# Optimization experiments

Measured on AMD Instinct MI355X. Metric: run time of the kernel, lower is better.

The kernel has to match this reference:

```python
import math
import jax, jax.numpy as jnp
import numpy as np

NUM_LAYERS = 4
D_MODEL = 1024
N_HEAD = 8
HEAD_DIM = D_MODEL // N_HEAD
B, L = 8, 512
EPS = 1e-5


def setup_inputs() -> dict:
    key = jax.random.key(0)
    ks = jax.random.split(key, 6)
    x = jax.random.normal(ks[0], (B, L, D_MODEL), dtype=jnp.float32)
    mask = jnp.ones((B, L), dtype=jnp.int32)
    qv_w = jax.random.normal(ks[1], (NUM_LAYERS, 2 * D_MODEL, D_MODEL), dtype=jnp.float32) * 0.02
    r_r_bias = jax.random.normal(ks[2], (NUM_LAYERS, N_HEAD, HEAD_DIM), dtype=jnp.float32) * 0.02
    r_w_bias = jax.random.normal(ks[3], (NUM_LAYERS, N_HEAD, HEAD_DIM), dtype=jnp.float32) * 0.02
    ffn_w = jax.random.normal(ks[4], (NUM_LAYERS, D_MODEL, D_MODEL), dtype=jnp.float32) * 0.02
    ffn_b = jnp.zeros((NUM_LAYERS, D_MODEL), dtype=jnp.float32)
    ln1_g = jnp.ones((NUM_LAYERS, D_MODEL), dtype=jnp.float32)
    ln1_b = jnp.zeros((NUM_LAYERS, D_MODEL), dtype=jnp.float32)
    ln2_g = jnp.ones((NUM_LAYERS, D_MODEL), dtype=jnp.float32)
    ln2_b = jnp.zeros((NUM_LAYERS, D_MODEL), dtype=jnp.float32)
    return dict(x=x, mask=mask, qv_w=qv_w, r_r_bias=r_r_bias, r_w_bias=r_w_bias,
                ln1_g=ln1_g, ln1_b=ln1_b, ffn_w=ffn_w, ffn_b=ffn_b,
                ln2_g=ln2_g, ln2_b=ln2_b)


def _rel_pos_embed(seq_len, dim):
    # weights[p + origin_shift] encodes sinusoid of relative position p;
    # selected positions are arange(-seq_len, seq_len) -> shape [2L, dim]
    half = dim // 2
    inv_freq = jnp.exp(jnp.arange(half, dtype=jnp.float32) * (-math.log(10000.0) / (half - 1)))
    pos = jnp.arange(-seq_len, seq_len, dtype=jnp.float32)
    ang = pos[:, None] * inv_freq[None, :]
    return jnp.concatenate([jnp.sin(ang), jnp.cos(ang)], axis=1)  # [2L, dim]


def _shift(BD):
    # [b,n,L,2L] -> [b,n,L,L] Transformer-XL shift trick
    b, n, l, _ = BD.shape
    BD = jnp.concatenate([BD, jnp.zeros((b, n, l, 1), BD.dtype)], axis=-1)
    BD = BD.reshape(b, n, -1, l)[:, :, :-1].reshape(b, n, l, -1)
    return BD[:, :, :, l:]


def _layernorm(x, g, b):
    mu = jnp.mean(x, axis=-1, keepdims=True)
    var = jnp.mean(jnp.square(x - mu), axis=-1, keepdims=True)
    return (x - mu) * jax.lax.rsqrt(var + EPS) * g + b


def _rel_attn(x, mask, qv_w, rr, rw, pe):
    b, l, d = x.shape
    qv = x @ qv_w.T                      # [b,l,2d]
    q, v = jnp.split(qv, 2, axis=-1)
    q = q.reshape(b, l, N_HEAD, HEAD_DIM).transpose(0, 2, 1, 3)
    k = x.reshape(b, l, N_HEAD, HEAD_DIM).transpose(0, 2, 1, 3)  # raw x as keys (per source)
    v = v.reshape(b, l, N_HEAD, HEAD_DIM).transpose(0, 2, 1, 3)
    AC = jnp.einsum('bnqd,bnkd->bnqk', q + rr[:, None], k)
    D_ = jnp.einsum('nd,ld->nl', rw, pe)[None, :, None]          # [1,n,1,2L]
    B_ = jnp.einsum('bnqd,ld->bnql', q, pe)                      # [b,n,L,2L]
    BD = _shift(B_ + D_)
    attn = AC + BD                                               # scale = 1
    attn = jnp.where(mask[:, None, None, :] == 0, -jnp.inf, attn)
    attn = jax.nn.softmax(attn, axis=-1)
    out = jnp.einsum('bnqk,bnkd->bqnd', attn, v).reshape(b, l, d)
    return out


def reference(x, mask, qv_w, r_r_bias, r_w_bias, ln1_g, ln1_b, ffn_w, ffn_b, ln2_g, ln2_b):
    pe = _rel_pos_embed(x.shape[1], HEAD_DIM)
    h = x
    for i in range(NUM_LAYERS):
        res = h
        h = _rel_attn(h, mask, qv_w[i], r_r_bias[i], r_w_bias[i], pe)
        h = _layernorm(h + res, ln1_g[i], ln1_b[i])
        res = h
        h = jax.nn.relu(h @ ffn_w[i].T + ffn_b[i])
        h = _layernorm(res + h, ln2_g[i], ln2_b[i])
    return h
```

## Files before the change

### kernel.cpp

```cpp
#include <hip/hip_runtime.h>
#include <math.h>

#define NL 4
#define DM 1024
#define NH 8
#define HD 128
#define BB 8
#define LL 512
#define MM (BB*LL)
#define PEN (2*LL)
#define QT 64
#define KT 32
#define NKT (LL/KT)
#define VS 44

typedef __attribute__((ext_vector_type(8))) __bf16 bf16x8;
typedef __attribute__((ext_vector_type(4))) float f32x4;

__device__ __forceinline__ unsigned short f2b(float f) {
  unsigned int u = __float_as_uint(f);
  u = (u + 0x7FFFu + ((u >> 16) & 1u)) >> 16;
  return (unsigned short)u;
}
__device__ __forceinline__ float b2f(unsigned short s) {
  return __uint_as_float(((unsigned int)s) << 16);
}
__device__ __forceinline__ void glds16(const void* g, void* l) {
  __builtin_amdgcn_global_load_lds(
      (const __attribute__((address_space(1))) unsigned int*)g,
      (__attribute__((address_space(3))) unsigned int*)l, 16, 0, 0);
}
union U8 { unsigned short s[8]; bf16x8 v; };
__device__ __forceinline__ void split8(const float4& a, const float4& b,
                                       bf16x8& h, bf16x8& l) {
  float x[8] = {a.x,a.y,a.z,a.w,b.x,b.y,b.z,b.w};
  U8 uh, ul;
#pragma unroll
  for (int e = 0; e < 8; ++e) {
    unsigned u = __float_as_uint(x[e]);
    uh.s[e] = (unsigned short)(u >> 16);
    ul.s[e] = f2b(x[e] - __uint_as_float(u & 0xffff0000u));
  }
  h = uh.v; l = ul.v;
}

__global__ __launch_bounds__(256) void pe_kernel(unsigned short* __restrict__ peh,
                                                 unsigned short* __restrict__ pel) {
  int idx = blockIdx.x * 256 + threadIdx.x;
  if (idx >= PEN * HD) return;
  int p = idx / HD, j = idx % HD;
  int tt = (j < 64) ? j : (j - 64);
  float invf = expf((float)tt * (-9.210340371976184f / 63.0f));
  float ang = (float)(p - LL) * invf;
  float v = (j < 64) ? sinf(ang) : cosf(ang);
  unsigned short h = f2b(v);
  peh[idx] = h;
  pel[idx] = f2b(v - b2f(h));
}

__global__ __launch_bounds__(256) void d2_kernel(const float* __restrict__ rrb,
                                                 const float* __restrict__ rwb,
                                                 const unsigned short* __restrict__ peh,
                                                 const unsigned short* __restrict__ pel,
                                                 float* __restrict__ d2) {
  int idx = blockIdx.x * 256 + threadIdx.x;
  if (idx >= NH * PEN) return;
  int n = idx / PEN, p = idx % PEN;
  float s = 0.f;
  for (int d = 0; d < HD; ++d) {
    float pv = b2f(peh[p*HD + d]) + b2f(pel[p*HD + d]);
    s += (rwb[n*HD + d] - rrb[n*HD + d]) * pv;
  }
  d2[idx] = s;
}

__global__ __launch_bounds__(256) void split_kernel(const float* __restrict__ in,
                                                    unsigned short* __restrict__ hi,
                                                    unsigned short* __restrict__ lo,
                                                    int n) {
  int i = (blockIdx.x * 256 + threadIdx.x) * 4;
  if (i >= n) return;
  float4 v = *(const float4*)&in[i];
  float x[4] = {v.x, v.y, v.z, v.w};
  ushort4 h4, l4;
  unsigned short* hp = (unsigned short*)&h4;
  unsigned short* lp = (unsigned short*)&l4;
#pragma unroll
  for (int e = 0; e < 4; ++e) {
    unsigned short h = f2b(x[e]);
    hp[e] = h;
    lp[e] = f2b(x[e] - b2f(h));
  }
  *(ushort4*)&hi[i] = h4;
  *(ushort4*)&lo[i] = l4;
}

template<bool FFN>
__global__ __launch_bounds__(256) void gemm_mfma(
    const unsigned short* __restrict__ Ah, const unsigned short* __restrict__ Al,
    const float* __restrict__ Bw, const float* __restrict__ bias,
    float* __restrict__ C, int N, int K, int ldc) {
  __shared__ __align__(16) unsigned short AsH[128*32];
  __shared__ __align__(16) unsigned short AsL[128*32];
  __shared__ __align__(16) unsigned short BsH[128*40];
  __shared__ __align__(16) unsigned short BsL[128*40];
  const int t = threadIdx.x;
  const int w = t >> 6, l = t & 63;
  const int bm = blockIdx.y * 128, bn = blockIdx.x * 128;
  const int wr = (w >> 1) * 64, wc = (w & 1) * 64;

  const unsigned short* Ahb = Ah + (size_t)(bm + (t >> 2)) * K + (t & 3) * 8;
  const unsigned short* Alb = Al + (size_t)(bm + (t >> 2)) * K + (t & 3) * 8;
  unsigned short* AsHw0 = &AsH[w * 512];
  unsigned short* AsHw1 = &AsH[2048 + w * 512];
  unsigned short* AsLw0 = &AsL[w * 512];
  unsigned short* AsLw1 = &AsL[2048 + w * 512];

  const int brow = t >> 1, bhalf = (t & 1) * 16;
  const float* Bb = Bw + (size_t)(bn + brow) * K + bhalf;

  f32x4 acc[4][4] = {};
  const int lm = l & 15;
  const int lk = (l >> 4) * 8;

  for (int k0 = 0; k0 < K; k0 += 32) {
    float4 bv[4];
#pragma unroll
    for (int c = 0; c < 4; ++c)
      bv[c] = *(const float4*)(Bb + k0 + c*4);
    glds16(Ahb + k0,                 AsHw0);
    glds16(Ahb + (size_t)64*K + k0,  AsHw1);
    glds16(Alb + k0,                 AsLw0);
    glds16(Alb + (size_t)64*K + k0,  AsLw1);
#pragma unroll
    for (int c = 0; c < 4; ++c) {
      float xs[4] = {bv[c].x, bv[c].y, bv[c].z, bv[c].w};
      ushort4 h4, l4;
      unsigned short* hp = (unsigned short*)&h4;
      unsigned short* lp = (unsigned short*)&l4;
#pragma unroll
      for (int e = 0; e < 4; ++e) {
        unsigned u = __float_as_uint(xs[e]);
        hp[e] = (unsigned short)(u >> 16);
        float r = xs[e] - __uint_as_float(u & 0xffff0000u);
        lp[e] = (unsigned short)(__float_as_uint(r) >> 16);
      }
      *(ushort4*)&BsH[brow*40 + bhalf + c*4] = h4;
      *(ushort4*)&BsL[brow*40 + bhalf + c*4] = l4;
    }
    __syncthreads();

    bf16x8 afh[4], afl[4], bfh[4], bfl[4];
#pragma unroll
    for (int i = 0; i < 4; ++i) {
      afh[i] = *(const bf16x8*)&AsH[(wr + i*16 + lm) * 32 + lk];
      afl[i] = *(const bf16x8*)&AsL[(wr + i*16 + lm) * 32 + lk];
    }
#pragma unroll
    for (int j = 0; j < 4; ++j) {
      bfh[j] = *(const bf16x8*)&BsH[(wc + j*16 + lm) * 40 + lk];
      bfl[j] = *(const bf16x8*)&BsL[(wc + j*16 + lm) * 40 + lk];
    }
#pragma unroll
    for (int i = 0; i < 4; ++i)
#pragma unroll
      for (int j = 0; j < 4; ++j) {
        acc[i][j] = __builtin_amdgcn_mfma_f32_16x16x32_bf16(afh[i], bfh[j], acc[i][j], 0, 0, 0);
        acc[i][j] = __builtin_amdgcn_mfma_f32_16x16x32_bf16(afh[i], bfl[j], acc[i][j], 0, 0, 0);
        acc[i][j] = __builtin_amdgcn_mfma_f32_16x16x32_bf16(afl[i], bfh[j], acc[i][j], 0, 0, 0);
      }
    __syncthreads();
  }

  const int cr = (l >> 4) * 4;
#pragma unroll
  for (int i = 0; i < 4; ++i) {
#pragma unroll
    for (int j = 0; j < 4; ++j) {
      int row = bm + wr + i*16 + cr;
      int col = bn + wc + j*16 + lm;
      float bvl = FFN ? bias[col] : 0.f;
      f32x4 a = acc[i][j];
#pragma unroll
      for (int r4 = 0; r4 < 4; ++r4) {
        float v = a[r4];
        if (FFN) v = fmaxf(v + bvl, 0.f);
        C[(size_t)(row + r4) * ldc + col] = v;
      }
    }
  }
}

__global__ __launch_bounds__(256, 2) void attn_mfma(
    const float* __restrict__ qv,
    const unsigned short* __restrict__ khp,
    const unsigned short* __restrict__ klp,
    const unsigned short* __restrict__ pehp,
    const unsigned short* __restrict__ pelp,
    const float* __restrict__ rrb,
    const int*   __restrict__ mask,
    const float* __restrict__ d2p,
    float* __restrict__ outp)
{
  __shared__ __align__(16) unsigned short KsH[KT*136];
  __shared__ __align__(16) unsigned short KsL[KT*136];
  __shared__ __align__(16) unsigned short VtH[HD*VS];
  __shared__ __align__(16) unsigned short VtL[HD*VS];
  __shared__ __align__(16) unsigned short PsH[4][16*40];
  __shared__ __align__(16) unsigned short PsL[4][16*40];

  const int q0 = blockIdx.x * QT;
  const int n  = blockIdx.y, b = blockIdx.z;
  const int t  = threadIdx.x;
  const int w  = t >> 6, l = t & 63;
  const int lm = l & 15, lg = l >> 4;
  const int q0w = q0 + w*16;
  const int r8 = t >> 3, s8 = t & 7;
  const int vr0 = t >> 5, vd4 = (t & 31)*4;

  bf16x8 qah[4], qal[4];
  {
    size_t qrow = (size_t)(b*LL + q0w + lm) * (2*DM) + (size_t)n*HD;
#pragma unroll
    for (int c = 0; c < 4; ++c) {
      int d0 = c*32 + lg*8;
      float4 x1 = *(const float4*)&qv[qrow + d0];
      float4 x2 = *(const float4*)&qv[qrow + d0 + 4];
      float4 r1 = *(const float4*)&rrb[n*HD + d0];
      float4 r2 = *(const float4*)&rrb[n*HD + d0 + 4];
      float4 a = {x1.x+r1.x, x1.y+r1.y, x1.z+r1.z, x1.w+r1.w};
      float4 bq = {x2.x+r2.x, x2.y+r2.y, x2.z+r2.z, x2.w+r2.w};
      split8(a, bq, qah[c], qal[c]);
    }
  }

  {
    size_t krow = (size_t)(b*LL + r8)*DM + (size_t)n*HD + s8*16;
    *(uint4*)&KsH[r8*136 + s8*16]     = *(const uint4*)&khp[krow];
    *(uint4*)&KsH[r8*136 + s8*16 + 8] = *(const uint4*)&khp[krow + 8];
    *(uint4*)&KsL[r8*136 + s8*16]     = *(const uint4*)&klp[krow];
    *(uint4*)&KsL[r8*136 + s8*16 + 8] = *(const uint4*)&klp[krow + 8];
    float4 vv[4];
#pragma unroll
    for (int i = 0; i < 4; ++i)
      vv[i] = *(const float4*)&qv[(size_t)(b*LL + vr0*4 + i)*(2*DM) + DM + n*HD + vd4];
#pragma unroll
    for (int e = 0; e < 4; ++e) {
      float xs[4] = {((const float*)&vv[0])[e], ((const float*)&vv[1])[e],
                     ((const float*)&vv[2])[e], ((const float*)&vv[3])[e]};
      ushort4 h4, l4;
      unsigned short* hp = (unsigned short*)&h4;
      unsigned short* lp = (unsigned short*)&l4;
#pragma unroll
      for (int i = 0; i < 4; ++i) {
        unsigned u = __float_as_uint(xs[i]);
        hp[i] = (unsigned short)(u >> 16);
        lp[i] = f2b(xs[i] - __uint_as_float(u & 0xffff0000u));
      }
      *(ushort4*)&VtH[(vd4+e)*VS + vr0*4] = h4;
      *(ushort4*)&VtL[(vd4+e)*VS + vr0*4] = l4;
    }
  }
  __syncthreads();

  float m_run[4] = {-3.0e38f, -3.0e38f, -3.0e38f, -3.0e38f};
  float l_run[4] = {0.f, 0.f, 0.f, 0.f};
  f32x4 accO[8] = {};
  f32x4 accB0 = {}, accB1 = {}, accB2 = {};

  for (int kt = 0; kt < NKT; ++kt) {
    const int k0 = kt * KT;
    const int base_w = k0 - q0w + 497;

    uint4 kxh0, kxh1, kxl0, kxl1;
    float4 vx[4];
    const bool pf = kt < NKT-1;
    if (pf) {
      size_t krow = (size_t)(b*LL + k0 + KT + r8)*DM + (size_t)n*HD + s8*16;
      kxh0 = *(const uint4*)&khp[krow];     kxh1 = *(const uint4*)&khp[krow + 8];
      kxl0 = *(const uint4*)&klp[krow];     kxl1 = *(const uint4*)&klp[krow + 8];
#pragma unroll
      for (int i = 0; i < 4; ++i)
        vx[i] = *(const float4*)&qv[(size_t)(b*LL + k0 + KT + vr0*4 + i)*(2*DM) + DM + n*HD + vd4];
    }

    float d2v1, d2v2;
    {
      int di1 = base_w + 16 + lm; di1 = di1 > PEN-1 ? PEN-1 : di1;
      int di2 = base_w + 32 + lm; di2 = di2 > PEN-1 ? PEN-1 : di2;
      d2v1 = d2p[n*PEN + di1];
      d2v2 = d2p[n*PEN + di2];
    }
    const int msk0 = mask[b*LL + k0 + lm];
    const int msk1 = mask[b*LL + k0 + 16 + lm];

    bf16x8 p1h[4], p1l[4], p2h[4], p2l[4];
    {
      int pr1 = base_w + 16 + lm; pr1 = pr1 > PEN-1 ? PEN-1 : pr1;
      int pr2 = base_w + 32 + lm; pr2 = pr2 > PEN-1 ? PEN-1 : pr2;
      const unsigned short* pb1 = pehp + (size_t)pr1*HD + lg*8;
      const unsigned short* pq1 = pelp + (size_t)pr1*HD + lg*8;
      const unsigned short* pb2 = pehp + (size_t)pr2*HD + lg*8;
      const unsigned short* pq2 = pelp + (size_t)pr2*HD + lg*8;
#pragma unroll
      for (int c = 0; c < 4; ++c) {
        p1h[c] = *(const bf16x8*)(pb1 + c*32);
        p1l[c] = *(const bf16x8*)(pq1 + c*32);
        p2h[c] = *(const bf16x8*)(pb2 + c*32);
        p2l[c] = *(const bf16x8*)(pq2 + c*32);
      }
    }

    f32x4 accA[2] = {};
#pragma unroll
    for (int tt = 0; tt < 2; ++tt)
#pragma unroll
      for (int c = 0; c < 4; ++c) {
        const int krow = tt*16 + lm;
        bf16x8 kfh = *(const bf16x8*)&KsH[krow*136 + (c*4+lg)*8];
        bf16x8 kfl = *(const bf16x8*)&KsL[krow*136 + (c*4+lg)*8];
        accA[tt] = __builtin_amdgcn_mfma_f32_16x16x32_bf16(qah[c], kfh, accA[tt], 0, 0, 0);
        accA[tt] = __builtin_amdgcn_mfma_f32_16x16x32_bf16(qah[c], kfl, accA[tt], 0, 0, 0);
        accA[tt] = __builtin_amdgcn_mfma_f32_16x16x32_bf16(qal[c], kfh, accA[tt], 0, 0, 0);
      }

    if (kt == 0) {
      int pr0 = base_w + lm; pr0 = pr0 > PEN-1 ? PEN-1 : pr0;
      const unsigned short* pb0 = pehp + (size_t)pr0*HD + lg*8;
      const unsigned short* pq0 = pelp + (size_t)pr0*HD + lg*8;
      f32x4 a = {};
#pragma unroll
      for (int c = 0; c < 4; ++c) {
        bf16x8 ph = *(const bf16x8*)(pb0 + c*32);
        bf16x8 pl = *(const bf16x8*)(pq0 + c*32);
        a = __builtin_amdgcn_mfma_f32_16x16x32_bf16(qah[c], ph, a, 0, 0, 0);
        a = __builtin_amdgcn_mfma_f32_16x16x32_bf16(qah[c], pl, a, 0, 0, 0);
        a = __builtin_amdgcn_mfma_f32_16x16x32_bf16(qal[c], ph, a, 0, 0, 0);
      }
      float dv0 = d2p[n*PEN + pr0];
#pragma unroll
      for (int r = 0; r < 4; ++r) a[r] += dv0;
      accB0 = a;
    } else {
      accB0 = accB2;
    }
    {
      f32x4 a = {};
#pragma unroll
      for (int c = 0; c < 4; ++c) {
        a = __builtin_amdgcn_mfma_f32_16x16x32_bf16(qah[c], p1h[c], a, 0, 0, 0);
        a = __builtin_amdgcn_mfma_f32_16x16x32_bf16(qah[c], p1l[c], a, 0, 0, 0);
        a = __builtin_amdgcn_mfma_f32_16x16x32_bf16(qal[c], p1h[c], a, 0, 0, 0);
      }
#pragma unroll
      for (int r = 0; r < 4; ++r) a[r] += d2v1;
      accB1 = a;
    }
    {
      f32x4 a = {};
#pragma unroll
      for (int c = 0; c < 4; ++c) {
        a = __builtin_amdgcn_mfma_f32_16x16x32_bf16(qah[c], p2h[c], a, 0, 0, 0);
        a = __builtin_amdgcn_mfma_f32_16x16x32_bf16(qah[c], p2l[c], a, 0, 0, 0);
        a = __builtin_amdgcn_mfma_f32_16x16x32_bf16(qal[c], p2h[c], a, 0, 0, 0);
      }
#pragma unroll
      for (int r = 0; r < 4; ++r) a[r] += d2v2;
      accB2 = a;
    }

    float s[2][4];
#pragma unroll
    for (int r = 0; r < 4; ++r) {
      const int qi = lg*4 + r;
      const int jm = (lm - qi + 15) & 15;
      const int src = (l & 48) | jm;
      const bool carry = lm > qi;
      float sh0 = __shfl(accB0[r], src);
      float sh1 = __shfl(accB1[r], src);
      float sh2 = __shfl(accB2[r], src);
      float bd0 = carry ? sh1 : sh0;
      float bd1 = carry ? sh2 : sh1;
      float v0 = accA[0][r] + bd0;
      float v1 = accA[1][r] + bd1;
      s[0][r] = (msk0 == 0) ? -1e30f : v0;
      s[1][r] = (msk1 == 0) ? -1e30f : v1;
    }

    float sc4[4];
#pragma unroll
    for (int r = 0; r < 4; ++r) {
      float mt = fmaxf(s[0][r], s[1][r]);
      mt = fmaxf(mt, __shfl_xor(mt, 1));
      mt = fmaxf(mt, __shfl_xor(mt, 2));
      mt = fmaxf(mt, __shfl_xor(mt, 4));
      mt = fmaxf(mt, __shfl_xor(mt, 8));
      float mn = fmaxf(m_run[r], mt);
      sc4[r] = __expf(m_run[r] - mn);
      m_run[r] = mn;
      float p0 = __expf(s[0][r] - mn);
      float p1 = __expf(s[1][r] - mn);
      s[0][r] = p0; s[1][r] = p1;
      float la = p0 + p1;
      la += __shfl_xor(la, 1);
      la += __shfl_xor(la, 2);
      la += __shfl_xor(la, 4);
      la += __shfl_xor(la, 8);
      l_run[r] = l_run[r]*sc4[r] + la;
    }
#pragma unroll
    for (int j8 = 0; j8 < 8; ++j8)
#pragma unroll
      for (int r = 0; r < 4; ++r)
        accO[j8][r] *= sc4[r];

#pragma unroll
    for (int tt = 0; tt < 2; ++tt)
#pragma unroll
      for (int r = 0; r < 4; ++r) {
        int qi = lg*4 + r, kc = tt*16 + lm;
        float p = s[tt][r];
        unsigned u = __float_as_uint(p);
        PsH[w][qi*40 + kc] = (unsigned short)(u >> 16);
        PsL[w][qi*40 + kc] = f2b(p - __uint_as_float(u & 0xffff0000u));
      }
    asm volatile("s_waitcnt lgkmcnt(0)" ::: "memory");
    __builtin_amdgcn_sched_barrier(0);

    {
      bf16x8 pah = *(const bf16x8*)&PsH[w][lm*40 + lg*8];
      bf16x8 pal = *(const bf16x8*)&PsL[w][lm*40 + lg*8];
#pragma unroll
      for (int j8 = 0; j8 < 8; ++j8) {
        const int dim = j8*16 + lm;
        bf16x8 vfh = *(const bf16x8*)&VtH[dim*VS + lg*8];
        bf16x8 vfl = *(const bf16x8*)&VtL[dim*VS + lg*8];
        accO[j8] = __builtin_amdgcn_mfma_f32_16x16x32_bf16(pah, vfh, accO[j8], 0, 0, 0);
        accO[j8] = __builtin_amdgcn_mfma_f32_16x16x32_bf16(pah, vfl, accO[j8], 0, 0, 0);
        accO[j8] = __builtin_amdgcn_mfma_f32_16x16x32_bf16(pal, vfh, accO[j8], 0, 0, 0);
      }
    }

    __syncthreads();

    if (pf) {
      *(uint4*)&KsH[r8*136 + s8*16]     = kxh0;
      *(uint4*)&KsH[r8*136 + s8*16 + 8] = kxh1;
      *(uint4*)&KsL[r8*136 + s8*16]     = kxl0;
      *(uint4*)&KsL[r8*136 + s8*16 + 8] = kxl1;
#pragma unroll
      for (int e = 0; e < 4; ++e) {
        float xs[4] = {((const float*)&vx[0])[e], ((const float*)&vx[1])[e],
                       ((const float*)&vx[2])[e], ((const float*)&vx[3])[e]};
        ushort4 h4, l4;
        unsigned short* hp = (unsigned short*)&h4;
        unsigned short* lp = (unsigned short*)&l4;
#pragma unroll
        for (int i = 0; i < 4; ++i) {
          unsigned u = __float_as_uint(xs[i]);
          hp[i] = (unsigned short)(u >> 16);
          lp[i] = f2b(xs[i] - __uint_as_float(u & 0xffff0000u));
        }
        *(ushort4*)&VtH[(vd4+e)*VS + vr0*4] = h4;
        *(ushort4*)&VtL[(vd4+e)*VS + vr0*4] = l4;
      }
    }
    __syncthreads();
  }

  float inv[4];
#pragma unroll
  for (int r = 0; r < 4; ++r) inv[r] = 1.0f / l_run[r];
#pragma unroll
  for (int j8 = 0; j8 < 8; ++j8)
#pragma unroll
    for (int r = 0; r < 4; ++r)
      outp[(size_t)(b*LL + q0w + lg*4 + r)*(2*DM) + n*HD + j8*16 + lm] = accO[j8][r] * inv[r];
}

__global__ __launch_bounds__(256) void add_ln_kernel(
    const float* __restrict__ y, int ys,
    const float* __restrict__ res,
    const float* __restrict__ g, const float* __restrict__ bt,
    float* __restrict__ out,
    unsigned short* __restrict__ ohi, unsigned short* __restrict__ olo)
{
  const int r = blockIdx.x, t = threadIdx.x;
  float4 v = *(const float4*)&y[(size_t)r*ys + t*4];
  float4 w = *(const float4*)&res[(size_t)r*DM + t*4];
  float4 s = {v.x+w.x, v.y+w.y, v.z+w.z, v.w+w.w};
  float sum = s.x + s.y + s.z + s.w;
  float ssq = s.x*s.x + s.y*s.y + s.z*s.z + s.w*s.w;
#pragma unroll
  for (int off = 32; off >= 1; off >>= 1) {
    sum += __shfl_down(sum, off);
    ssq += __shfl_down(ssq, off);
  }
  __shared__ float red[8];
  int wid = t >> 6;
  if ((t & 63) == 0) { red[wid] = sum; red[wid+4] = ssq; }
  __syncthreads();
  float totS = red[0] + red[1] + red[2] + red[3];
  float totQ = red[4] + red[5] + red[6] + red[7];
  float mu  = totS * (1.0f/DM);
  float var = totQ * (1.0f/DM) - mu*mu;
  float inv = rsqrtf(var + 1e-5f);
  float4 gg = *(const float4*)&g[t*4];
  float4 bb = *(const float4*)&bt[t*4];
  float4 o;
  o.x = (s.x - mu)*inv*gg.x + bb.x;
  o.y = (s.y - mu)*inv*gg.y + bb.y;
  o.z = (s.z - mu)*inv*gg.z + bb.z;
  o.w = (s.w - mu)*inv*gg.w + bb.w;
  *(float4*)&out[(size_t)r*DM + t*4] = o;
  float xs[4] = {o.x, o.y, o.z, o.w};
  ushort4 h4, l4;
  unsigned short* hp = (unsigned short*)&h4;
  unsigned short* lp = (unsigned short*)&l4;
#pragma unroll
  for (int e = 0; e < 4; ++e) {
    unsigned short h = f2b(xs[e]);
    hp[e] = h;
    lp[e] = f2b(xs[e] - b2f(h));
  }
  *(ushort4*)&ohi[(size_t)r*DM + t*4] = h4;
  *(ushort4*)&olo[(size_t)r*DM + t*4] = l4;
}

extern "C" void kernel_launch(void* const* d_in, const int* in_sizes, int n_in,
                              void* d_out, int out_size, void* d_ws, size_t ws_size,
                              hipStream_t stream) {
  const float* x    = (const float*)d_in[0];
  const int*   mask = (const int*)d_in[1];
  const float* qv_w = (const float*)d_in[2];
  const float* rrb  = (const float*)d_in[3];
  const float* rwb  = (const float*)d_in[4];
  const float* ln1g = (const float*)d_in[5];
  const float* ln1b = (const float*)d_in[6];
  const float* ffnw = (const float*)d_in[7];
  const float* ffnb = (const float*)d_in[8];
  const float* ln2g = (const float*)d_in[9];
  const float* ln2b = (const float*)d_in[10];

  float* h  = (float*)d_out;
  unsigned short* peh = (unsigned short*)d_ws;
  unsigned short* pel = peh + (size_t)PEN*HD;
  float* d2  = (float*)(pel + (size_t)PEN*HD);
  float* qv  = d2 + (size_t)NH*PEN;
  unsigned short* hhi = (unsigned short*)(qv + (size_t)MM*2*DM);
  unsigned short* hlo = hhi + (size_t)MM*DM;

  hipMemcpyAsync(h, x, (size_t)MM*DM*sizeof(float), hipMemcpyDeviceToDevice, stream);
  split_kernel<<<(MM*DM)/1024, 256, 0, stream>>>(x, hhi, hlo, MM*DM);
  pe_kernel<<<(PEN*HD)/256, 256, 0, stream>>>(peh, pel);

  for (int l = 0; l < NL; ++l) {
    const float* rr_l = rrb + (size_t)l*NH*HD;
    const float* rw_l = rwb + (size_t)l*NH*HD;
    d2_kernel<<<(NH*PEN)/256, 256, 0, stream>>>(rr_l, rw_l, peh, pel, d2);
    gemm_mfma<false><<<dim3((2*DM)/128, MM/128), 256, 0, stream>>>(
        hhi, hlo, qv_w + (size_t)l*2*DM*DM, nullptr, qv, 2*DM, DM, 2*DM);
    attn_mfma<<<dim3(LL/QT, NH, BB), 256, 0, stream>>>(
        qv, hhi, hlo, peh, pel, rr_l, mask, d2, qv);
    add_ln_kernel<<<MM, 256, 0, stream>>>(qv, 2*DM, h,
        ln1g + (size_t)l*DM, ln1b + (size_t)l*DM, h, hhi, hlo);
    gemm_mfma<true><<<dim3(DM/128, MM/128), 256, 0, stream>>>(
        hhi, hlo, ffnw + (size_t)l*DM*DM, ffnb + (size_t)l*DM, qv + DM, DM, DM, 2*DM);
    add_ln_kernel<<<MM, 256, 0, stream>>>(qv + DM, 2*DM, h,
        ln2g + (size_t)l*DM, ln2b + (size_t)l*DM, h, hhi, hlo);
  }
  (void)in_sizes; (void)n_in; (void)out_size; (void)ws_size;
}
```

Measured before the change: 1.077 ms.

## Deepen GEMM K-tile with swizzled LDS, remap workgroups, skip redundant softmax rescale

The split-bf16 GEMM now stages 64-wide K slices instead of 32, halving the number of loop iterations and barriers. The A tile in LDS uses an XOR swizzle in place of padding to avoid bank conflicts. Workgroup IDs are remapped so neighbouring blocks share tiles in cache. In the attention kernel, the online-softmax rescale of the output accumulators and running sum is skipped when no row max grew in the wavefront. The cost is more LDS per block, which may lower occupancy, plus a wave-wide vote and branch.

```diff
diff --git a/kernel.cpp b/kernel.cpp
--- a/kernel.cpp
+++ b/kernel.cpp
@@ -100,40 +100,42 @@
     const unsigned short* __restrict__ Ah, const unsigned short* __restrict__ Al,
     const float* __restrict__ Bw, const float* __restrict__ bias,
     float* __restrict__ C, int N, int K, int ldc) {
-  __shared__ __align__(16) unsigned short AsH[128*32];
-  __shared__ __align__(16) unsigned short AsL[128*32];
-  __shared__ __align__(16) unsigned short BsH[128*40];
-  __shared__ __align__(16) unsigned short BsL[128*40];
+  __shared__ __align__(16) unsigned short AsH[128*64];
+  __shared__ __align__(16) unsigned short AsL[128*64];
+  __shared__ __align__(16) unsigned short BsH[128*72];
+  __shared__ __align__(16) unsigned short BsL[128*72];
   const int t = threadIdx.x;
   const int w = t >> 6, l = t & 63;
-  const int bm = blockIdx.y * 128, bn = blockIdx.x * 128;
+  const int gx = gridDim.x;
+  const int nwg = gx * gridDim.y;
+  const int id = blockIdx.y * gx + blockIdx.x;
+  const int swz = (id & 7) * (nwg >> 3) + (id >> 3);
+  const int bm = (swz / gx) * 128, bn = (swz % gx) * 128;
   const int wr = (w >> 1) * 64, wc = (w & 1) * 64;
 
-  const unsigned short* Ahb = Ah + (size_t)(bm + (t >> 2)) * K + (t & 3) * 8;
-  const unsigned short* Alb = Al + (size_t)(bm + (t >> 2)) * K + (t & 3) * 8;
-  unsigned short* AsHw0 = &AsH[w * 512];
-  unsigned short* AsHw1 = &AsH[2048 + w * 512];
-  unsigned short* AsLw0 = &AsL[w * 512];
-  unsigned short* AsLw1 = &AsL[2048 + w * 512];
-
-  const int brow = t >> 1, bhalf = (t & 1) * 16;
+  const int aseg = ((t & 7) ^ ((t >> 3) & 7)) * 8;
+  const unsigned short* Ahb = Ah + (size_t)(bm + (t >> 3)) * K + aseg;
+  const unsigned short* Alb = Al + (size_t)(bm + (t >> 3)) * K + aseg;
+
+  const int brow = t >> 1, bhalf = (t & 1) * 32;
   const float* Bb = Bw + (size_t)(bn + brow) * K + bhalf;
 
   f32x4 acc[4][4] = {};
   const int lm = l & 15;
-  const int lk = (l >> 4) * 8;
-
-  for (int k0 = 0; k0 < K; k0 += 32) {
-    float4 bv[4];
-#pragma unroll
-    for (int c = 0; c < 4; ++c)
+  const int lg = l >> 4;
+
+  for (int k0 = 0; k0 < K; k0 += 64) {
+    float4 bv[8];
+#pragma unroll
+    for (int c = 0; c < 8; ++c)
       bv[c] = *(const float4*)(Bb + k0 + c*4);
-    glds16(Ahb + k0,                 AsHw0);
-    glds16(Ahb + (size_t)64*K + k0,  AsHw1);
-    glds16(Alb + k0,                 AsLw0);
-    glds16(Alb + (size_t)64*K + k0,  AsLw1);
-#pragma unroll
-    for (int c = 0; c < 4; ++c) {
+#pragma unroll
+    for (int i = 0; i < 4; ++i) {
+      glds16(Ahb + (size_t)(i*32)*K + k0, &AsH[w*512 + i*2048]);
+      glds16(Alb + (size_t)(i*32)*K + k0, &AsL[w*512 + i*2048]);
+    }
+#pragma unroll
+    for (int c = 0; c < 8; ++c) {
       float xs[4] = {bv[c].x, bv[c].y, bv[c].z, bv[c].w};
       ushort4 h4, l4;
       unsigned short* hp = (unsigned short*)&h4;
@@ -145,30 +147,35 @@
         float r = xs[e] - __uint_as_float(u & 0xffff0000u);
         lp[e] = (unsigned short)(__float_as_uint(r) >> 16);
       }
-      *(ushort4*)&BsH[brow*40 + bhalf + c*4] = h4;
-      *(ushort4*)&BsL[brow*40 + bhalf + c*4] = l4;
+      *(ushort4*)&BsH[brow*72 + bhalf + c*4] = h4;
+      *(ushort4*)&BsL[brow*72 + bhalf + c*4] = l4;
     }
     __syncthreads();
 
-    bf16x8 afh[4], afl[4], bfh[4], bfl[4];
-#pragma unroll
-    for (int i = 0; i < 4; ++i) {
-      afh[i] = *(const bf16x8*)&AsH[(wr + i*16 + lm) * 32 + lk];
-      afl[i] = *(const bf16x8*)&AsL[(wr + i*16 + lm) * 32 + lk];
-    }
-#pragma unroll
-    for (int j = 0; j < 4; ++j) {
-      bfh[j] = *(const bf16x8*)&BsH[(wc + j*16 + lm) * 40 + lk];
-      bfl[j] = *(const bf16x8*)&BsL[(wc + j*16 + lm) * 40 + lk];
-    }
-#pragma unroll
-    for (int i = 0; i < 4; ++i)
+#pragma unroll
+    for (int kk = 0; kk < 2; ++kk) {
+      bf16x8 afh[4], afl[4], bfh[4], bfl[4];
+#pragma unroll
+      for (int i = 0; i < 4; ++i) {
+        const int row = wr + i*16 + lm;
+        const int sw = ((kk*4 + lg) ^ (lm & 7)) * 8;
+        afh[i] = *(const bf16x8*)&AsH[row*64 + sw];
+        afl[i] = *(const bf16x8*)&AsL[row*64 + sw];
+      }
 #pragma unroll
       for (int j = 0; j < 4; ++j) {
-        acc[i][j] = __builtin_amdgcn_mfma_f32_16x16x32_bf16(afh[i], bfh[j], acc[i][j], 0, 0, 0);
-        acc[i][j] = __builtin_amdgcn_mfma_f32_16x16x32_bf16(afh[i], bfl[j], acc[i][j], 0, 0, 0);
-        acc[i][j] = __builtin_amdgcn_mfma_f32_16x16x32_bf16(afl[i], bfh[j], acc[i][j], 0, 0, 0);
-      }
+        bfh[j] = *(const bf16x8*)&BsH[(wc + j*16 + lm)*72 + kk*32 + lg*8];
+        bfl[j] = *(const bf16x8*)&BsL[(wc + j*16 + lm)*72 + kk*32 + lg*8];
+      }
+#pragma unroll
+      for (int i = 0; i < 4; ++i)
+#pragma unroll
+        for (int j = 0; j < 4; ++j) {
+          acc[i][j] = __builtin_amdgcn_mfma_f32_16x16x32_bf16(afh[i], bfh[j], acc[i][j], 0, 0, 0);
+          acc[i][j] = __builtin_amdgcn_mfma_f32_16x16x32_bf16(afh[i], bfl[j], acc[i][j], 0, 0, 0);
+          acc[i][j] = __builtin_amdgcn_mfma_f32_16x16x32_bf16(afl[i], bfh[j], acc[i][j], 0, 0, 0);
+        }
+    }
     __syncthreads();
   }
 
@@ -387,7 +394,8 @@
       s[1][r] = (msk1 == 0) ? -1e30f : v1;
     }
 
-    float sc4[4];
+    float mt4[4];
+    int allold = 1;
 #pragma unroll
     for (int r = 0; r < 4; ++r) {
       float mt = fmaxf(s[0][r], s[1][r]);
@@ -395,24 +403,32 @@
       mt = fmaxf(mt, __shfl_xor(mt, 2));
       mt = fmaxf(mt, __shfl_xor(mt, 4));
       mt = fmaxf(mt, __shfl_xor(mt, 8));
-      float mn = fmaxf(m_run[r], mt);
-      sc4[r] = __expf(m_run[r] - mn);
-      m_run[r] = mn;
-      float p0 = __expf(s[0][r] - mn);
-      float p1 = __expf(s[1][r] - mn);
+      mt4[r] = mt;
+      allold &= (mt <= m_run[r]) ? 1 : 0;
+    }
+    if (!__all(allold)) {
+#pragma unroll
+      for (int r = 0; r < 4; ++r) {
+        float mn = fmaxf(m_run[r], mt4[r]);
+        float sc = __expf(m_run[r] - mn);
+        m_run[r] = mn;
+        l_run[r] *= sc;
+#pragma unroll
+        for (int j8 = 0; j8 < 8; ++j8) accO[j8][r] *= sc;
+      }
+    }
+#pragma unroll
+    for (int r = 0; r < 4; ++r) {
+      float p0 = __expf(s[0][r] - m_run[r]);
+      float p1 = __expf(s[1][r] - m_run[r]);
       s[0][r] = p0; s[1][r] = p1;
       float la = p0 + p1;
       la += __shfl_xor(la, 1);
       la += __shfl_xor(la, 2);
       la += __shfl_xor(la, 4);
       la += __shfl_xor(la, 8);
-      l_run[r] = l_run[r]*sc4[r] + la;
-    }
-#pragma unroll
-    for (int j8 = 0; j8 < 8; ++j8)
-#pragma unroll
-      for (int r = 0; r < 4; ++r)
-        accO[j8][r] *= sc4[r];
+      l_run[r] += la;
+    }
 
 #pragma unroll
     for (int tt = 0; tt < 2; ++tt)
```

New measurement: 1.023 ms. 1.05x faster.
